# Performance work log

Measured on AMD Instinct MI355X. Metric: run time of the kernel, lower is better.

Reference implementation:

```python
import jax, jax.numpy as jnp
import numpy as np

NW = 30000   # window nodes
NE = 30000   # example nodes
E  = 480000  # edges per relation (avg degree 16)
H  = 512     # hidden_channels
L  = 4       # num_layers
SLOPE = 0.2
LAM = 0.5    # CSRA residual attention weight


def _segment_mean(x, idx, n):
    s = jax.ops.segment_sum(x, idx, num_segments=n)
    c = jax.ops.segment_sum(jnp.ones((idx.shape[0], 1), x.dtype), idx, num_segments=n)
    return s / jnp.maximum(c, 1.0)


def _sage(x_src, x_dst, edge, Wl, Wr, b, n_dst):
    # PyG SAGEConv: lin_l(mean_agg(x_j)) + lin_r(x_i)
    agg = _segment_mean(x_src[edge[0]], edge[1], n_dst)  # [n_dst, H]
    return agg @ Wl + b + x_dst @ Wr


def setup_inputs() -> dict:
    key = jax.random.key(0)
    ks = jax.random.split(key, 24)
    s = 0.02
    nrm = lambda k, shape: (jax.random.normal(k, shape, jnp.float32) * s)
    return {
        "x_window": jax.random.normal(ks[0], (NW, 1949), jnp.float32),
        "x_example": jax.random.normal(ks[1], (NE, 100), jnp.float32),
        "edge_near": jax.random.randint(ks[2], (2, E), 0, NW, jnp.int32),
        "edge_close": jax.random.randint(ks[3], (2, E), 0, NE, jnp.int32),
        "edge_refer": jax.random.randint(ks[4], (2, E), 0, NW, jnp.int32),  # src=example, dst=window
        "W_win": nrm(ks[5], (1949, H)),
        "W_exp": nrm(ks[6], (100, H)),
        "W_post": nrm(ks[7], (H, H)),
        "W_ey": nrm(ks[8], (250, H)),
        "Wl_near": nrm(ks[9], (L, H, H)),
        "Wr_near": nrm(ks[10], (L, H, H)),
        "b_near": jnp.zeros((L, H), jnp.float32),
        "Wl_close": nrm(ks[11], (L, H, H)),
        "Wr_close": nrm(ks[12], (L, H, H)),
        "b_close": jnp.zeros((L, H), jnp.float32),
        "Wl_refer": nrm(ks[13], (L, H, H)),
        "Wr_refer": nrm(ks[14], (L, H, H)),
        "b_refer": jnp.zeros((L, H), jnp.float32),
        "w_pool": nrm(ks[15], (H,)),
        "W_lin": nrm(ks[16], (H, 100)),
        "b_lin": jnp.zeros((100,), jnp.float32),
    }


def reference(x_window, x_example, edge_near, edge_close, edge_refer,
              W_win, W_exp, W_post, W_ey,
              Wl_near, Wr_near, b_near,
              Wl_close, Wr_close, b_close,
              Wl_refer, Wr_refer, b_refer,
              w_pool, W_lin, b_lin):
    lrelu = lambda x: jax.nn.leaky_relu(x, SLOPE)
    post = lambda h: lrelu(lrelu(h) @ W_post)  # LeakyReLU -> Linear -> LeakyReLU

    h_exp = post(x_example @ W_exp)            # [NE, H]
    h_win = post(x_window @ W_win)             # [NW, H]
    # example_y is computed in the original but dropped by HeteroConv (no conv
    # targets it); compute for faithfulness, unused.
    _example_y = h_exp[:, -250:] @ W_ey

    for l in range(L):
        o_near = _sage(h_win, h_win, edge_near, Wl_near[l], Wr_near[l], b_near[l], NW)
        o_refer = _sage(h_exp, h_win, edge_refer, Wl_refer[l], Wr_refer[l], b_refer[l], NW)
        o_close = _sage(h_exp, h_exp, edge_close, Wl_close[l], Wr_close[l], b_close[l], NE)
        h_win = lrelu((o_near + o_refer) * 0.5)  # HeteroConv aggr='mean' over 2 relations
        h_exp = lrelu(o_close)

    # CSRA-style pooling: residual attention over 'refer' edges into window nodes
    src, dst = edge_refer[0], edge_refer[1]
    score = h_exp @ w_pool                      # [NE]
    s = score[src]                              # [E]
    m = jax.ops.segment_max(s, dst, num_segments=NW)
    ex = jnp.exp(s - m[dst])
    z = jax.ops.segment_sum(ex, dst, num_segments=NW)
    att = ex / jnp.maximum(z[dst], 1e-12)
    pooled = jax.ops.segment_sum(att[:, None] * h_exp[src], dst, num_segments=NW)
    out = h_win + LAM * pooled                  # [NW, H]
    return out @ W_lin + b_lin                  # [NW, 100]
```

## Files before the change

### kernel.cpp

```cpp
#include <hip/hip_runtime.h>
#include <hip/hip_bf16.h>
#include <cstdint>
#include <cstddef>

#define NW 30000
#define NE 30000
#define EE 480000
#define HD 512
#define NL 4
#define SLOPE 0.2f
#define LAM 0.5f
#define ROWP 30080
#define MT 235
#define WHH ((size_t)HD * HD)

typedef short short8 __attribute__((ext_vector_type(8)));
typedef float f32x4 __attribute__((ext_vector_type(4)));

static __device__ __forceinline__ float lrelu_f(float x){
    return fmaxf(x, 0.f) + SLOPE * fminf(x, 0.f);
}
static __device__ __forceinline__ short f2bf(float f){
    uint32_t u = __builtin_bit_cast(uint32_t, f);
    u += 0x7FFFu + ((u >> 16) & 1u);
    return (short)(u >> 16);
}
static __device__ __forceinline__ float bf2f(short s){
    uint32_t u = ((uint32_t)(uint16_t)s) << 16;
    return __builtin_bit_cast(float, u);
}

typedef const __attribute__((address_space(1))) void* gas_t;
typedef __attribute__((address_space(3))) void* las_t;
static __device__ __forceinline__ void gload16(const void* g, void* l){
    __builtin_amdgcn_global_load_lds((gas_t)g, (las_t)l, 16, 0, 0);
}


__global__ void count3_kernel(const int* __restrict__ dn, const int* __restrict__ dr,
                              const int* __restrict__ dc, int* __restrict__ deg){
    int z = blockIdx.y;
    const int* dst = (z == 0) ? dn : ((z == 1) ? dr : dc);
    int e = blockIdx.x * 256 + threadIdx.x;
    if (e < EE) atomicAdd(&deg[z * 30000 + dst[e]], 1);
}

__global__ void scan3_kernel(const int* __restrict__ deg, int* __restrict__ off3){
    const int* dg = deg + blockIdx.x * 30000;
    int* off = off3 + blockIdx.x * (NW + 1);
    int n = 30000;
    __shared__ int tmp[1024];
    int t = threadIdx.x;
    int carry = 0;
    if (t == 0) off[0] = 0;
    for (int base = 0; base < n; base += 1024){
        int v = (base + t < n) ? dg[base + t] : 0;
        tmp[t] = v; __syncthreads();
        for (int d = 1; d < 1024; d <<= 1){
            int add = (t >= d) ? tmp[t - d] : 0;
            __syncthreads();
            tmp[t] += add;
            __syncthreads();
        }
        if (base + t < n) off[base + t + 1] = tmp[t] + carry;
        carry += tmp[1023];
        __syncthreads();
    }
}

__global__ void fill3_kernel(const int* __restrict__ sn, const int* __restrict__ dn,
                             const int* __restrict__ sr, const int* __restrict__ dr,
                             const int* __restrict__ sc, const int* __restrict__ dc,
                             int* __restrict__ cur, const int* __restrict__ off3,
                             int* __restrict__ el3){
    int z = blockIdx.y;
    const int* src = (z == 0) ? sn : ((z == 1) ? sr : sc);
    const int* dst = (z == 0) ? dn : ((z == 1) ? dr : dc);
    const int* off = off3 + z * (NW + 1);
    int* el = el3 + (size_t)z * EE;
    int e = blockIdx.x * 256 + threadIdx.x;
    if (e < EE){
        int d = dst[e];
        int p = atomicAdd(&cur[z * 30000 + d], 1);
        el[off[d] + p] = src[e];
    }
}


__global__ __launch_bounds__(256)
void transpose_bf_kernel(const float* __restrict__ in, short* __restrict__ out,
                         int K, int N, int Kpad){
    __shared__ float tile[32][33];
    int kbase = blockIdx.y * 32, nbase = blockIdx.x * 32;
    int tx = threadIdx.x & 31, ty = threadIdx.x >> 5;
    #pragma unroll
    for (int r = 0; r < 4; ++r){
        int k = kbase + ty + r * 8;
        float v = 0.f;
        if (k < K) v = in[(size_t)k * N + nbase + tx];
        tile[ty + r * 8][tx] = v;
    }
    __syncthreads();
    #pragma unroll
    for (int r = 0; r < 4; ++r){
        int n = nbase + ty + r * 8;
        int k = kbase + tx;
        if (k < Kpad) out[(size_t)n * Kpad + k] = f2bf(tile[tx][ty + r * 8]);
    }
}


__global__ __launch_bounds__(256)
void transpose_all_kernel(const float* __restrict__ Wln, const float* __restrict__ Wlr,
                          const float* __restrict__ Wlc, const float* __restrict__ Wrc,
                          const float* __restrict__ Wrn, const float* __restrict__ Wrr,
                          const float* __restrict__ Wpost, short* __restrict__ outT){
    __shared__ float tile[32][33];
    int z = blockIdx.z;
    const float* a; const float* b = nullptr;
    if (z < 4) a = Wln + (size_t)z * WHH;
    else if (z < 8) a = Wlr + (size_t)(z - 4) * WHH;
    else if (z < 12) a = Wlc + (size_t)(z - 8) * WHH;
    else if (z < 16) a = Wrc + (size_t)(z - 12) * WHH;
    else if (z < 20){ a = Wrn + (size_t)(z - 16) * WHH; b = Wrr + (size_t)(z - 16) * WHH; }
    else a = Wpost;
    short* outp = outT + (size_t)z * WHH;
    int kbase = blockIdx.y * 32, nbase = blockIdx.x * 32;
    int tx = threadIdx.x & 31, ty = threadIdx.x >> 5;
    #pragma unroll
    for (int r = 0; r < 4; ++r){
        int k = kbase + ty + r * 8;
        float v = a[(size_t)k * HD + nbase + tx];
        if (b) v += b[(size_t)k * HD + nbase + tx];
        tile[ty + r * 8][tx] = v;
    }
    __syncthreads();
    #pragma unroll
    for (int r = 0; r < 4; ++r){
        int n = nbase + ty + r * 8;
        outp[(size_t)n * HD + kbase + tx] = f2bf(tile[tx][ty + r * 8]);
    }
}

__global__ void addf_kernel(const float* __restrict__ a, const float* __restrict__ b,
                            float* __restrict__ o, int n){
    int i = blockIdx.x * 256 + threadIdx.x;
    if (i < n) o[i] = a[i] + b[i];
}


__global__ __launch_bounds__(256)
void conv_xw_kernel(const float* __restrict__ x, short* __restrict__ o){
    int idx = blockIdx.x * 256 + threadIdx.x;
    if (idx >= 30000 * 244) return;
    int row = idx / 244, c8 = idx - row * 244;
    int base = c8 * 8;
    short8 v = {};
    const float* xp = x + (size_t)row * 1949 + base;
    if (base + 8 <= 1949){
        f32x4 a = *(const f32x4*)xp;
        f32x4 bq = *(const f32x4*)(xp + 4);
        #pragma unroll
        for (int j = 0; j < 4; ++j){ v[j] = f2bf(a[j]); v[j + 4] = f2bf(bq[j]); }
    } else {
        #pragma unroll
        for (int j = 0; j < 8; ++j) if (base + j < 1949) v[j] = f2bf(xp[j]);
    }
    *(short8*)(o + (size_t)row * 1952 + base) = v;
}


__global__ __launch_bounds__(256)
void conv_xe_kernel(const float* __restrict__ x, short* __restrict__ o){
    int idx = blockIdx.x * 256 + threadIdx.x;
    if (idx >= ROWP * 16) return;
    int row = idx >> 4, c8 = idx & 15;
    int base = c8 * 8;
    short8 v = {};
    if (row < 30000){
        const float* xp = x + (size_t)row * 100 + base;
        #pragma unroll
        for (int j = 0; j < 8; ++j) if (base + j < 100) v[j] = f2bf(xp[j]);
    }
    *(short8*)(o + (size_t)row * 128 + base) = v;
}


__global__ __launch_bounds__(256)
void seg_mean3_kernel(const short* __restrict__ hw, const short* __restrict__ he,
                      const int* __restrict__ off3, const int* __restrict__ el3,
                      short* __restrict__ aggA, short* __restrict__ aggB, short* __restrict__ aggC){
    int slot = blockIdx.x * 4 + (threadIdx.x >> 6);
    int lane = threadIdx.x & 63;
    if (slot >= 3 * NW) return;
    int seg = slot / NW;
    int dst = slot - seg * NW;
    const short* h = (seg == 0) ? hw : he;
    const int* off = off3 + seg * (NW + 1);
    const int* el = el3 + (size_t)seg * EE;
    short* out = (seg == 0) ? aggA : ((seg == 1) ? aggB : aggC);
    int s0 = off[dst], s1 = off[dst + 1];
    float acc[8] = {};
    int e = s0;
    for (; e + 8 <= s1; e += 8){
        int idx[8];
        #pragma unroll
        for (int u = 0; u < 8; ++u) idx[u] = el[e + u];
        short8 v[8];
        #pragma unroll
        for (int u = 0; u < 8; ++u) v[u] = *(const short8*)(h + (size_t)idx[u] * HD + lane * 8);
        #pragma unroll
        for (int u = 0; u < 8; ++u)
            #pragma unroll
            for (int j = 0; j < 8; ++j) acc[j] += bf2f(v[u][j]);
    }
    for (; e < s1; ++e){
        short8 v = *(const short8*)(h + (size_t)el[e] * HD + lane * 8);
        #pragma unroll
        for (int j = 0; j < 8; ++j) acc[j] += bf2f(v[j]);
    }
    float inv = (s1 > s0) ? 1.0f / (float)(s1 - s0) : 0.0f;
    short8 o8;
    #pragma unroll
    for (int j = 0; j < 8; ++j) o8[j] = f2bf(acc[j] * inv);
    *(short8*)(out + (size_t)dst * HD + lane * 8) = o8;
}


template<int DUAL>
__global__ __launch_bounds__(256)
void mgemm2_kernel(
    const short* __restrict__ a00, const short* __restrict__ a01, const short* __restrict__ a02,
    const short* __restrict__ b00, const short* __restrict__ b01, const short* __restrict__ b02,
    const float* __restrict__ bias0, short* __restrict__ c160, float* __restrict__ c320,
    int np0, int kt0, int act0,
    const short* __restrict__ a10, const short* __restrict__ a11, const short* __restrict__ a12,
    const short* __restrict__ b10, const short* __restrict__ b11, const short* __restrict__ b12,
    const float* __restrict__ bias1, short* __restrict__ c161, float* __restrict__ c321,
    int np1, int kt1, int act1,
    int mreal){
    __shared__ short lds[24576];

    int nwg = gridDim.x, orig = blockIdx.x;
    int q = nwg >> 3, r = nwg & 7;
    int xcd = orig & 7, lid = orig >> 3;
    int logical = (xcd < r ? xcd * (q + 1) : r * (q + 1) + (xcd - r) * q) + lid;
    int mtile = logical >> 2, nc = logical & 3;
    int dsel, ml;
    if (DUAL){ dsel = mtile & 1; ml = mtile >> 1; } else { dsel = 0; ml = mtile; }

    const short* A0 = dsel ? a10 : a00;
    const short* A1 = dsel ? a11 : a01;
    const short* A2 = dsel ? a12 : a02;
    const short* B0 = dsel ? b10 : b00;
    const short* B1 = dsel ? b11 : b01;
    const short* B2 = dsel ? b12 : b02;
    const float* bias = dsel ? bias1 : bias0;
    short* C16 = dsel ? c161 : c160;
    float* C32 = dsel ? c321 : c320;
    const int np = dsel ? np1 : np0;
    const int kt = dsel ? kt1 : kt0;
    const int act = dsel ? act1 : act0;

    const int row0 = ml * 128, n0 = nc * 128;
    const int t = threadIdx.x, wid = t >> 6, lane = t & 63;
    const int wm = (wid >> 1) * 64, wn = (wid & 1) * 64;
    const int lg = lane >> 4, lr = lane & 15;
    f32x4 acc[4][4] = {};

    int rowi[2], ci[2];
    #pragma unroll
    for (int i = 0; i < 2; ++i){
        int sl = i * 256 + t;
        rowi[i] = sl >> 2;
        ci[i] = (sl & 3) ^ ((rowi[i] >> 1) & 3);
    }
    const int kpt = kt >> 5;
    const int nsteps = np * kpt;

    const short* Acur = A0;
    const short* Bcur = B0;
    int sk = 0, sp = 0, sbuf = 0;

    auto stage = [&](){
        int k0 = sk * 32;
        #pragma unroll
        for (int i = 0; i < 2; ++i){
            int ao = (row0 + rowi[i]) * kt + k0 + ci[i] * 8;
            gload16(Acur + ao, &lds[sbuf * 4096 + (i * 256 + wid * 64) * 8]);
        }
        #pragma unroll
        for (int i = 0; i < 2; ++i){
            int bo = (n0 + rowi[i]) * kt + k0 + ci[i] * 8;
            gload16(Bcur + bo, &lds[12288 + sbuf * 4096 + (i * 256 + wid * 64) * 8]);
        }
        sbuf = (sbuf == 2) ? 0 : sbuf + 1;
        if (++sk == kpt){
            sk = 0; ++sp;
            Acur = (sp == 1) ? A1 : A2;
            Bcur = (sp == 1) ? B1 : B2;
        }
    };
    auto compute = [&](int cb){
        const char* baseA = (const char*)(lds + cb * 4096);
        const char* baseB = (const char*)(lds + 12288 + cb * 4096);
        short8 af[4], bfr[4];
        #pragma unroll
        for (int f = 0; f < 4; ++f){
            int rowA = wm + f * 16 + lr;
            af[f] = *(const short8*)(baseA + rowA * 64 + ((lg ^ ((rowA >> 1) & 3)) << 4));
            int rowB = wn + f * 16 + lr;
            bfr[f] = *(const short8*)(baseB + rowB * 64 + ((lg ^ ((rowB >> 1) & 3)) << 4));
        }
        #pragma unroll
        for (int i = 0; i < 4; ++i)
            #pragma unroll
            for (int j = 0; j < 4; ++j)
                acc[i][j] = __builtin_amdgcn_mfma_f32_16x16x32_bf16(af[i], bfr[j], acc[i][j], 0, 0, 0);
    };

    stage();
    int cbuf = 0;
    for (int s = 0; s < nsteps; ++s){
        if (s + 1 < nsteps){
            stage();
            asm volatile("s_waitcnt vmcnt(4)" ::: "memory");
        } else {
            asm volatile("s_waitcnt vmcnt(0)" ::: "memory");
        }
        __builtin_amdgcn_s_barrier();
        __builtin_amdgcn_sched_barrier(0);
        compute(cbuf);
        cbuf = (cbuf == 2) ? 0 : cbuf + 1;
    }

    float bv[4];
    #pragma unroll
    for (int f = 0; f < 4; ++f) bv[f] = bias ? bias[n0 + wn + f * 16 + lr] : 0.f;
    #pragma unroll
    for (int i = 0; i < 4; ++i){
        #pragma unroll
        for (int r2 = 0; r2 < 4; ++r2){
            int gr = row0 + wm + i * 16 + lg * 4 + r2;
            #pragma unroll
            for (int j = 0; j < 4; ++j){
                int gc = n0 + wn + j * 16 + lr;
                float v = acc[i][j][r2] + bv[j];
                if (act == 2) v *= 0.5f;
                if (act) v = lrelu_f(v);
                C16[(size_t)gr * HD + gc] = f2bf(v);
                if (C32 && gr < mreal) C32[(size_t)gr * HD + gc] = v;
            }
        }
    }
}


__global__ __launch_bounds__(128)
void mgemm_af32_kernel(const float* __restrict__ A0, const short* __restrict__ B0,
                       short* __restrict__ C16, int M){
    constexpr int KT = 1952, KACT = 1949, KPT = KT / 32, NSTEPS = KPT, N = 512;
    __shared__ short ldsA[2][2048];
    __shared__ short ldsB[2][4096];
    int nwg = gridDim.x;
    int orig = blockIdx.x;
    int q = nwg >> 3, r = nwg & 7;
    int xcd = orig & 7, lid = orig >> 3;
    int logical = (xcd < r ? xcd * (q + 1) : r * (q + 1) + (xcd - r) * q) + lid;
    const int m0 = (logical >> 2) * 64, n0 = (logical & 3) * 128;
    const int t = threadIdx.x, wid = t >> 6, lane = t & 63;
    const int wn = wid * 64;
    const int lg = lane >> 4, lr = lane & 15;
    f32x4 acc[4][4] = {};
    int rowiA[2], ciA[2];
    #pragma unroll
    for (int i = 0; i < 2; ++i){
        int sl = i * 128 + t;
        rowiA[i] = sl >> 2;
        ciA[i] = (sl & 3) ^ ((rowiA[i] >> 1) & 3);
    }
    int rowiB[4], ciB[4];
    #pragma unroll
    for (int i = 0; i < 4; ++i){
        int sl = i * 128 + t;
        rowiB[i] = sl >> 2;
        ciB[i] = (sl & 3) ^ ((rowiB[i] >> 1) & 3);
    }
    f32x4 ra[2][2];
    auto stage_load = [&](int s){
        int k0 = s * 32;
        int bb = s & 1;
        #pragma unroll
        for (int i = 0; i < 2; ++i){
            int gr = m0 + rowiA[i];
            int gk = k0 + ciA[i] * 8;
            ra[i][0] = (f32x4){0,0,0,0};
            ra[i][1] = (f32x4){0,0,0,0};
            if (gr < M){
                const float* ap = A0 + (size_t)gr * KACT + gk;
                if (gk + 8 <= KACT){
                    ra[i][0] = *(const f32x4*)ap;
                    ra[i][1] = *(const f32x4*)(ap + 4);
                } else {
                    #pragma unroll
                    for (int j = 0; j < 8; ++j)
                        if (gk + j < KACT) ra[i][j >> 2][j & 3] = ap[j];
                }
            }
        }
        #pragma unroll
        for (int i = 0; i < 4; ++i)
            gload16(B0 + (size_t)(n0 + rowiB[i]) * KT + k0 + ciB[i] * 8,
                    &ldsB[bb][(i * 128 + wid * 64) * 8]);
    };
    auto stage_writeA = [&](int s){
        int bb = s & 1;
        #pragma unroll
        for (int i = 0; i < 2; ++i){
            short8 v;
            #pragma unroll
            for (int j = 0; j < 8; ++j) v[j] = f2bf(ra[i][j >> 2][j & 3]);
            *(short8*)&ldsA[bb][(i * 128 + t) * 8] = v;
        }
    };
    auto compute = [&](int s){
        int bb = s & 1;
        short8 af[4], bfr[4];
        #pragma unroll
        for (int f = 0; f < 4; ++f){
            int rowA = f * 16 + lr;
            af[f] = *(const short8*)((const char*)&ldsA[bb][0] + rowA * 64 + ((lg ^ ((rowA >> 1) & 3)) << 4));
            int rowB = wn + f * 16 + lr;
            bfr[f] = *(const short8*)((const char*)&ldsB[bb][0] + rowB * 64 + ((lg ^ ((rowB >> 1) & 3)) << 4));
        }
        #pragma unroll
        for (int i = 0; i < 4; ++i)
            #pragma unroll
            for (int j = 0; j < 4; ++j)
                acc[i][j] = __builtin_amdgcn_mfma_f32_16x16x32_bf16(af[i], bfr[j], acc[i][j], 0, 0, 0);
    };
    stage_load(0);
    stage_writeA(0);
    __syncthreads();
    for (int s = 0; s < NSTEPS; ++s){
        if (s + 1 < NSTEPS) stage_load(s + 1);
        compute(s);
        if (s + 1 < NSTEPS) stage_writeA(s + 1);
        __syncthreads();
    }
    #pragma unroll
    for (int i = 0; i < 4; ++i){
        #pragma unroll
        for (int r2 = 0; r2 < 4; ++r2){
            int gr = m0 + i * 16 + lg * 4 + r2;
            if (gr >= M) continue;
            #pragma unroll
            for (int j = 0; j < 4; ++j){
                int gc = n0 + wn + j * 16 + lr;
                C16[(size_t)gr * N + gc] = f2bf(lrelu_f(acc[i][j][r2]));
            }
        }
    }
}


__global__ __launch_bounds__(256)
void gemm_kernel(const float* __restrict__ A, const float* __restrict__ B,
                 const float* __restrict__ bias, float* __restrict__ C,
                 int M, int N, int K){
    const int BM = 128, BN = 64, BK = 16;
    __shared__ float As[BK][BM];
    __shared__ float Bs[BK][BN];
    int m0 = blockIdx.y * BM, n0 = blockIdx.x * BN;
    int t = threadIdx.x;
    int tx = t & 15, ty = t >> 4;
    float acc[8][4] = {};
    for (int k0 = 0; k0 < K; k0 += BK){
        #pragma unroll
        for (int i = 0; i < 2; ++i){
            int idx = i * 256 + t;
            int row = idx >> 2, kg = idx & 3;
            float4 v = make_float4(0,0,0,0);
            int gr = m0 + row, gk = k0 + kg * 4;
            if (gr < M && gk + 4 <= K)
                v = *reinterpret_cast<const float4*>(A + (size_t)gr * K + gk);
            As[kg*4+0][row] = v.x; As[kg*4+1][row] = v.y;
            As[kg*4+2][row] = v.z; As[kg*4+3][row] = v.w;
        }
        {
            int row = t >> 4, cg = t & 15;
            int gk = k0 + row, col = n0 + cg * 4;
            float4 v = make_float4(0,0,0,0);
            if (gk < K){
                if (col + 4 <= N){
                    v = *reinterpret_cast<const float4*>(B + (size_t)gk * N + col);
                } else {
                    float tp[4] = {0,0,0,0};
                    #pragma unroll
                    for (int j = 0; j < 4; ++j) if (col + j < N) tp[j] = B[(size_t)gk * N + col + j];
                    v = make_float4(tp[0], tp[1], tp[2], tp[3]);
                }
            }
            *reinterpret_cast<float4*>(&Bs[row][cg*4]) = v;
        }
        __syncthreads();
        #pragma unroll
        for (int k = 0; k < BK; ++k){
            float a[8], b[4];
            #pragma unroll
            for (int r = 0; r < 8; ++r) a[r] = As[k][ty*8 + r];
            #pragma unroll
            for (int c = 0; c < 4; ++c) b[c] = Bs[k][tx*4 + c];
            #pragma unroll
            for (int r = 0; r < 8; ++r)
                #pragma unroll
                for (int c = 0; c < 4; ++c)
                    acc[r][c] = fmaf(a[r], b[c], acc[r][c]);
        }
        __syncthreads();
    }
    #pragma unroll
    for (int r = 0; r < 8; ++r){
        int gr = m0 + ty*8 + r;
        if (gr >= M) continue;
        #pragma unroll
        for (int c = 0; c < 4; ++c){
            int gc = n0 + tx*4 + c;
            if (gc >= N) continue;
            C[(size_t)gr * N + gc] = acc[r][c] + bias[gc];
        }
    }
}


__global__ void score_kernel(const short* __restrict__ he, const float* __restrict__ w,
                             float* __restrict__ score){
    int row = blockIdx.x * 4 + (threadIdx.x >> 6);
    int lane = threadIdx.x & 63;
    if (row >= NE) return;
    float s = 0.f;
    #pragma unroll
    for (int j = 0; j < 8; ++j){
        int idx = lane + j * 64;
        s += bf2f(he[(size_t)row * HD + idx]) * w[idx];
    }
    #pragma unroll
    for (int off = 32; off > 0; off >>= 1) s += __shfl_down(s, off);
    if (lane == 0) score[row] = s;
}

__global__ __launch_bounds__(256)
void pool_kernel(const short* __restrict__ he, const float* __restrict__ hwf,
                 const float* __restrict__ score, const int* __restrict__ off,
                 const int* __restrict__ elist, float* __restrict__ outp){
    int dst = blockIdx.x * 4 + (threadIdx.x >> 6);
    int lane = threadIdx.x & 63;
    if (dst >= NW) return;
    int s0 = off[dst], s1 = off[dst + 1];
    float m = -INFINITY;
    for (int e = s0 + lane; e < s1; e += 64) m = fmaxf(m, score[elist[e]]);
    #pragma unroll
    for (int o = 1; o < 64; o <<= 1) m = fmaxf(m, __shfl_xor(m, o));
    float z = 0.f;
    for (int e = s0 + lane; e < s1; e += 64) z += expf(score[elist[e]] - m);
    #pragma unroll
    for (int o = 1; o < 64; o <<= 1) z += __shfl_xor(z, o);
    float zinv = 1.0f / fmaxf(z, 1e-12f);

    float acc[8] = {};
    int e = s0;
    for (; e + 4 <= s1; e += 4){
        int idx[4]; float at[4];
        #pragma unroll
        for (int u = 0; u < 4; ++u) idx[u] = elist[e + u];
        #pragma unroll
        for (int u = 0; u < 4; ++u) at[u] = expf(score[idx[u]] - m) * zinv;
        #pragma unroll
        for (int u = 0; u < 4; ++u){
            short8 v = *(const short8*)(he + (size_t)idx[u] * HD + lane * 8);
            #pragma unroll
            for (int k = 0; k < 8; ++k) acc[k] += at[u] * bf2f(v[k]);
        }
    }
    for (; e < s1; ++e){
        int src = elist[e];
        float at = expf(score[src] - m) * zinv;
        short8 v = *(const short8*)(he + (size_t)src * HD + lane * 8);
        #pragma unroll
        for (int k = 0; k < 8; ++k) acc[k] += at * bf2f(v[k]);
    }
    f32x4 h0 = *(const f32x4*)(hwf + (size_t)dst * HD + lane * 8);
    f32x4 h1 = *(const f32x4*)(hwf + (size_t)dst * HD + lane * 8 + 4);
    f32x4 o0, o1;
    #pragma unroll
    for (int k = 0; k < 4; ++k){ o0[k] = h0[k] + LAM * acc[k]; o1[k] = h1[k] + LAM * acc[k+4]; }
    *(f32x4*)(outp + (size_t)dst * HD + lane * 8) = o0;
    *(f32x4*)(outp + (size_t)dst * HD + lane * 8 + 4) = o1;
}


extern "C" void kernel_launch(void* const* d_in, const int* in_sizes, int n_in,
                              void* d_out, int out_size, void* d_ws, size_t ws_size,
                              hipStream_t stream){
    const float* x_window = (const float*)d_in[0];
    const float* x_example= (const float*)d_in[1];
    const int*   e_near   = (const int*)d_in[2];
    const int*   e_close  = (const int*)d_in[3];
    const int*   e_refer  = (const int*)d_in[4];
    const float* W_win    = (const float*)d_in[5];
    const float* W_exp    = (const float*)d_in[6];
    const float* W_post   = (const float*)d_in[7];
    const float* Wl_near  = (const float*)d_in[9];
    const float* Wr_near  = (const float*)d_in[10];
    const float* b_near   = (const float*)d_in[11];
    const float* Wl_close = (const float*)d_in[12];
    const float* Wr_close = (const float*)d_in[13];
    const float* b_close  = (const float*)d_in[14];
    const float* Wl_refer = (const float*)d_in[15];
    const float* Wr_refer = (const float*)d_in[16];
    const float* b_refer  = (const float*)d_in[17];
    const float* w_pool   = (const float*)d_in[18];
    const float* W_lin    = (const float*)d_in[19];
    const float* b_lin    = (const float*)d_in[20];
    float* out = (float*)d_out;
    (void)in_sizes; (void)n_in; (void)out_size;

    char* w = (char*)d_ws;
    size_t o = 0;
    auto alloc = [&](size_t bytes)->char*{
        char* p = w + o;
        o += (bytes + 255) & ~(size_t)255;
        return p;
    };
    const size_t HBH = (size_t)ROWP * HD * 2;

    short* h16[2][2];
    h16[0][0] = (short*)alloc(HBH); h16[0][1] = (short*)alloc(HBH);
    h16[1][0] = (short*)alloc(HBH); h16[1][1] = (short*)alloc(HBH);
    short* aggA = (short*)alloc(HBH);
    short* aggB = (short*)alloc(HBH);
    short* aggC = (short*)alloc(HBH);
    float* hwf  = (float*)alloc((size_t)NW * HD * 4);
    float* pooled = (float*)alloc((size_t)NW * HD * 4);
    short* xe16   = (short*)alloc((size_t)ROWP * 128 * 2);
    short* WwinT  = (short*)alloc((size_t)HD * 1952 * 2);
    short* WexpT  = (short*)alloc((size_t)HD * 128 * 2);
    short* WT     = (short*)alloc((size_t)21 * WHH * 2);
    short* WlnT = WT;
    short* WlrT = WT + 4 * WHH;
    short* WlcT = WT + 8 * WHH;
    short* WrcT = WT + 12 * WHH;
    short* WcbT = WT + 16 * WHH;
    short* WpostT = WT + 20 * WHH;
    float* bsum   = (float*)alloc((size_t)NL * HD * 4);
    float* score  = (float*)alloc((size_t)NE * 4);
    int* degcur = (int*)alloc((size_t)6 * 30000 * 4);
    int* deg3 = degcur;
    int* cur3 = degcur + 90000;
    int* off3 = (int*)alloc((size_t)3 * (NW + 1) * 4);
    int* el3  = (int*)alloc((size_t)3 * EE * 4);
    int* off_r = off3 + (NW + 1);

    const size_t XWB = (size_t)ROWP * 1952 * 2;
    bool haveXW16 = false;
    short* xw16 = nullptr;
    size_t rem = (ws_size > o) ? ws_size - o : 0;
    if (rem >= XWB + 256){
        xw16 = (short*)alloc(XWB);
        haveXW16 = true;
    }

    const int* src_n = e_near;  const int* dst_n = e_near + EE;
    const int* src_c = e_close; const int* dst_c = e_close + EE;
    const int* src_r = e_refer; const int* dst_r = e_refer + EE;

    hipMemsetAsync(degcur, 0, (size_t)6 * 30000 * 4, stream);
    int eg = (EE + 255) / 256;
    hipLaunchKernelGGL(count3_kernel, dim3(eg, 3), dim3(256), 0, stream, dst_n, dst_r, dst_c, deg3);
    hipLaunchKernelGGL(scan3_kernel, dim3(3), dim3(1024), 0, stream, deg3, off3);
    hipLaunchKernelGGL(fill3_kernel, dim3(eg, 3), dim3(256), 0, stream,
                       src_n, dst_n, src_r, dst_r, src_c, dst_c, cur3, off3, el3);

    hipLaunchKernelGGL(transpose_bf_kernel, dim3(16, 61, 1), dim3(256), 0, stream,
                       W_win, WwinT, 1949, HD, 1952);
    hipLaunchKernelGGL(transpose_bf_kernel, dim3(16, 4, 1), dim3(256), 0, stream,
                       W_exp, WexpT, 100, HD, 128);
    hipLaunchKernelGGL(transpose_all_kernel, dim3(16, 16, 21), dim3(256), 0, stream,
                       Wl_near, Wl_refer, Wl_close, Wr_close, Wr_near, Wr_refer, W_post, WT);
    hipLaunchKernelGGL(addf_kernel, dim3((NL * HD + 255) / 256), dim3(256), 0, stream,
                       b_near, b_refer, bsum, NL * HD);
    hipLaunchKernelGGL(conv_xe_kernel, dim3((ROWP * 16 + 255) / 256), dim3(256), 0, stream,
                       x_example, xe16);
    if (haveXW16)
        hipLaunchKernelGGL(conv_xw_kernel, dim3((30000 * 244 + 255) / 256), dim3(256), 0, stream,
                           x_window, xw16);

    const short* z16 = xe16;
    const float* zf = nullptr;

    hipLaunchKernelGGL((mgemm2_kernel<0>), dim3(MT * 4), dim3(256), 0, stream,
        xe16, z16, z16, WexpT, z16, z16, zf, aggA, (float*)nullptr, 1, 128, 1,
        z16, z16, z16, z16, z16, z16, zf, (short*)nullptr, (float*)nullptr, 0, 32, 0, 30000);
    if (haveXW16){
        hipLaunchKernelGGL((mgemm2_kernel<0>), dim3(MT * 4), dim3(256), 0, stream,
            xw16, z16, z16, WwinT, z16, z16, zf, aggB, (float*)nullptr, 1, 1952, 1,
            z16, z16, z16, z16, z16, z16, zf, (short*)nullptr, (float*)nullptr, 0, 32, 0, 30000);
    } else {
        hipLaunchKernelGGL(mgemm_af32_kernel, dim3(4 * ((NW + 63) / 64)), dim3(128), 0, stream,
                           x_window, WwinT, aggB, NW);
    }
    hipLaunchKernelGGL((mgemm2_kernel<1>), dim3(2 * MT * 4), dim3(256), 0, stream,
        aggA, z16, z16, WpostT, z16, z16, zf, h16[1][0], (float*)nullptr, 1, 512, 1,
        aggB, z16, z16, WpostT, z16, z16, zf, h16[0][0], (float*)nullptr, 1, 512, 1, 30000);

    for (int l = 0; l < NL; ++l){
        int cur = l & 1, nxt = cur ^ 1;
        const short* wl_n = WlnT + (size_t)l * WHH;
        const short* wl_r = WlrT + (size_t)l * WHH;
        const short* wl_c = WlcT + (size_t)l * WHH;
        const short* wr_c = WrcT + (size_t)l * WHH;
        const short* wcb  = WcbT + (size_t)l * WHH;
        const float* bs   = bsum + (size_t)l * HD;
        const float* bc   = b_close + (size_t)l * HD;
        bool last = (l == NL - 1);

        hipLaunchKernelGGL(seg_mean3_kernel, dim3((3 * NW + 3) / 4), dim3(256), 0, stream,
                           h16[0][cur], h16[1][cur], off3, el3, aggA, aggB, aggC);
        hipLaunchKernelGGL((mgemm2_kernel<1>), dim3(2 * MT * 4), dim3(256), 0, stream,
            aggA, aggB, h16[0][cur], wl_n, wl_r, wcb, bs, h16[0][nxt],
            last ? hwf : (float*)nullptr, 3, 512, 2,
            aggC, h16[1][cur], z16, wl_c, wr_c, z16, bc, h16[1][nxt],
            (float*)nullptr, 2, 512, 1, 30000);
    }
    int fin = NL & 1;

    hipLaunchKernelGGL(score_kernel, dim3((NE + 3) / 4), dim3(256), 0, stream,
                       h16[1][fin], w_pool, score);
    hipLaunchKernelGGL(pool_kernel, dim3((NW + 3) / 4), dim3(256), 0, stream,
                       h16[1][fin], hwf, score, off_r, el3 + (size_t)EE, pooled);

    hipLaunchKernelGGL(gemm_kernel, dim3(2, (NW + 127) / 128), dim3(256), 0, stream,
                       pooled, W_lin, b_lin, out, NW, 100, HD);
}
```

Before: 1.763 ms.

## Overlap self-weight GEMMs with segment-mean gather in one fused launch

The self-term products (h_win·Wcb and h_exp·Wr_close) move into a new kernel that runs GEMM blocks and segment-mean gather blocks side by side in the same grid. This lets the compute-bound and memory-bound work share the GPU at once. The main layer GEMM then uses fewer K panels and adds the precomputed bf16 self-term in its epilogue. The mgemm2 pipeline is also changed to prefetch two stages ahead, and s_setprio is raised around the MFMA work. The cost is extra bf16 intermediate buffers, an added rounding step on the self-term, and a possible race risk in the 3-buffer prefetch now that the trailing barrier is gone.

```diff
diff --git a/kernel.cpp b/kernel.cpp
--- a/kernel.cpp
+++ b/kernel.cpp
@@ -187,43 +187,121 @@
 
 
 __global__ __launch_bounds__(256)
-void seg_mean3_kernel(const short* __restrict__ hw, const short* __restrict__ he,
-                      const int* __restrict__ off3, const int* __restrict__ el3,
-                      short* __restrict__ aggA, short* __restrict__ aggB, short* __restrict__ aggC){
-    int slot = blockIdx.x * 4 + (threadIdx.x >> 6);
-    int lane = threadIdx.x & 63;
-    if (slot >= 3 * NW) return;
-    int seg = slot / NW;
-    int dst = slot - seg * NW;
-    const short* h = (seg == 0) ? hw : he;
-    const int* off = off3 + seg * (NW + 1);
-    const int* el = el3 + (size_t)seg * EE;
-    short* out = (seg == 0) ? aggA : ((seg == 1) ? aggB : aggC);
-    int s0 = off[dst], s1 = off[dst + 1];
-    float acc[8] = {};
-    int e = s0;
-    for (; e + 8 <= s1; e += 8){
-        int idx[8];
-        #pragma unroll
-        for (int u = 0; u < 8; ++u) idx[u] = el[e + u];
-        short8 v[8];
-        #pragma unroll
-        for (int u = 0; u < 8; ++u) v[u] = *(const short8*)(h + (size_t)idx[u] * HD + lane * 8);
-        #pragma unroll
-        for (int u = 0; u < 8; ++u)
-            #pragma unroll
-            for (int j = 0; j < 8; ++j) acc[j] += bf2f(v[u][j]);
-    }
-    for (; e < s1; ++e){
-        short8 v = *(const short8*)(h + (size_t)el[e] * HD + lane * 8);
-        #pragma unroll
-        for (int j = 0; j < 8; ++j) acc[j] += bf2f(v[j]);
-    }
-    float inv = (s1 > s0) ? 1.0f / (float)(s1 - s0) : 0.0f;
-    short8 o8;
-    #pragma unroll
-    for (int j = 0; j < 8; ++j) o8[j] = f2bf(acc[j] * inv);
-    *(short8*)(out + (size_t)dst * HD + lane * 8) = o8;
+void fused_self_seg_kernel(const short* __restrict__ hw, const short* __restrict__ he,
+                           const short* __restrict__ Wcb, const short* __restrict__ Wrc,
+                           short* __restrict__ Zw16, short* __restrict__ Ze16,
+                           const int* __restrict__ off3, const int* __restrict__ el3,
+                           short* __restrict__ aggA, short* __restrict__ aggB,
+                           short* __restrict__ aggC, int ngemm){
+    __shared__ short lds[16384];
+    int t = threadIdx.x;
+    if ((int)blockIdx.x < ngemm){
+        int logical = blockIdx.x;
+        int mtile = logical >> 2, nc = logical & 3;
+        int dsel = mtile & 1, ml = mtile >> 1;
+        const short* A = dsel ? he : hw;
+        const short* B = dsel ? Wrc : Wcb;
+        short* C16 = dsel ? Ze16 : Zw16;
+        const int row0 = ml * 128, n0 = nc * 128;
+        const int wid = t >> 6, lane = t & 63;
+        const int wm = (wid >> 1) * 64, wn = (wid & 1) * 64;
+        const int lg = lane >> 4, lr = lane & 15;
+        f32x4 acc[4][4] = {};
+        int rowi[2], ci[2];
+        #pragma unroll
+        for (int i = 0; i < 2; ++i){
+            int sl = i * 256 + t;
+            rowi[i] = sl >> 2;
+            ci[i] = (sl & 3) ^ ((rowi[i] >> 1) & 3);
+        }
+        auto stage = [&](int s){
+            int k0 = s * 32, bb = s & 1;
+            #pragma unroll
+            for (int i = 0; i < 2; ++i)
+                gload16(A + (size_t)(row0 + rowi[i]) * HD + k0 + ci[i] * 8,
+                        &lds[bb * 4096 + (i * 256 + wid * 64) * 8]);
+            #pragma unroll
+            for (int i = 0; i < 2; ++i)
+                gload16(B + (size_t)(n0 + rowi[i]) * HD + k0 + ci[i] * 8,
+                        &lds[8192 + bb * 4096 + (i * 256 + wid * 64) * 8]);
+        };
+        auto compute = [&](int bb){
+            const char* baseA = (const char*)(lds + bb * 4096);
+            const char* baseB = (const char*)(lds + 8192 + bb * 4096);
+            short8 af[4], bfr[4];
+            #pragma unroll
+            for (int f = 0; f < 4; ++f){
+                int rowA = wm + f * 16 + lr;
+                af[f] = *(const short8*)(baseA + rowA * 64 + ((lg ^ ((rowA >> 1) & 3)) << 4));
+                int rowB = wn + f * 16 + lr;
+                bfr[f] = *(const short8*)(baseB + rowB * 64 + ((lg ^ ((rowB >> 1) & 3)) << 4));
+            }
+            #pragma unroll
+            for (int i = 0; i < 4; ++i)
+                #pragma unroll
+                for (int j = 0; j < 4; ++j)
+                    acc[i][j] = __builtin_amdgcn_mfma_f32_16x16x32_bf16(af[i], bfr[j], acc[i][j], 0, 0, 0);
+        };
+        stage(0);
+        for (int s = 0; s < 16; ++s){
+            if (s + 1 < 16){
+                stage(s + 1);
+                asm volatile("s_waitcnt vmcnt(4)" ::: "memory");
+            } else {
+                asm volatile("s_waitcnt vmcnt(0)" ::: "memory");
+            }
+            __builtin_amdgcn_s_barrier();
+            __builtin_amdgcn_sched_barrier(0);
+            compute(s & 1);
+            asm volatile("s_waitcnt lgkmcnt(0)" ::: "memory");
+            __builtin_amdgcn_sched_barrier(0);
+            __builtin_amdgcn_s_barrier();
+        }
+        #pragma unroll
+        for (int i = 0; i < 4; ++i)
+            #pragma unroll
+            for (int r2 = 0; r2 < 4; ++r2){
+                int gr = row0 + wm + i * 16 + lg * 4 + r2;
+                #pragma unroll
+                for (int j = 0; j < 4; ++j)
+                    C16[(size_t)gr * HD + n0 + wn + j * 16 + lr] = f2bf(acc[i][j][r2]);
+            }
+    } else {
+        int slot = (blockIdx.x - ngemm) * 4 + (t >> 6);
+        int lane = t & 63;
+        if (slot >= 3 * NW) return;
+        int seg = slot / NW;
+        int dst = slot - seg * NW;
+        const short* h = (seg == 0) ? hw : he;
+        const int* off = off3 + seg * (NW + 1);
+        const int* el = el3 + (size_t)seg * EE;
+        short* outp = (seg == 0) ? aggA : ((seg == 1) ? aggB : aggC);
+        int s0 = off[dst], s1 = off[dst + 1];
+        float acc[8] = {};
+        int e = s0;
+        for (; e + 8 <= s1; e += 8){
+            int idx[8];
+            #pragma unroll
+            for (int u = 0; u < 8; ++u) idx[u] = el[e + u];
+            short8 v[8];
+            #pragma unroll
+            for (int u = 0; u < 8; ++u) v[u] = *(const short8*)(h + (size_t)idx[u] * HD + lane * 8);
+            #pragma unroll
+            for (int u = 0; u < 8; ++u)
+                #pragma unroll
+                for (int j = 0; j < 8; ++j) acc[j] += bf2f(v[u][j]);
+        }
+        for (; e < s1; ++e){
+            short8 v = *(const short8*)(h + (size_t)el[e] * HD + lane * 8);
+            #pragma unroll
+            for (int j = 0; j < 8; ++j) acc[j] += bf2f(v[j]);
+        }
+        float inv = (s1 > s0) ? 1.0f / (float)(s1 - s0) : 0.0f;
+        short8 o8;
+        #pragma unroll
+        for (int j = 0; j < 8; ++j) o8[j] = f2bf(acc[j] * inv);
+        *(short8*)(outp + (size_t)dst * HD + lane * 8) = o8;
+    }
 }
 
 
@@ -233,11 +311,11 @@
     const short* __restrict__ a00, const short* __restrict__ a01, const short* __restrict__ a02,
     const short* __restrict__ b00, const short* __restrict__ b01, const short* __restrict__ b02,
     const float* __restrict__ bias0, short* __restrict__ c160, float* __restrict__ c320,
-    int np0, int kt0, int act0,
+    const short* __restrict__ cin0, int np0, int kt0, int act0,
     const short* __restrict__ a10, const short* __restrict__ a11, const short* __restrict__ a12,
     const short* __restrict__ b10, const short* __restrict__ b11, const short* __restrict__ b12,
     const float* __restrict__ bias1, short* __restrict__ c161, float* __restrict__ c321,
-    int np1, int kt1, int act1,
+    const short* __restrict__ cin1, int np1, int kt1, int act1,
     int mreal){
     __shared__ short lds[24576];
 
@@ -258,6 +336,7 @@
     const float* bias = dsel ? bias1 : bias0;
     short* C16 = dsel ? c161 : c160;
     float* C32 = dsel ? c321 : c320;
+    const short* cin = dsel ? cin1 : cin0;
     const int np = dsel ? np1 : np0;
     const int kt = dsel ? kt1 : kt0;
     const int act = dsel ? act1 : act0;
@@ -320,17 +399,19 @@
     };
 
     stage();
+    stage();
     int cbuf = 0;
     for (int s = 0; s < nsteps; ++s){
         if (s + 1 < nsteps){
-            stage();
             asm volatile("s_waitcnt vmcnt(4)" ::: "memory");
         } else {
             asm volatile("s_waitcnt vmcnt(0)" ::: "memory");
         }
         __builtin_amdgcn_s_barrier();
-        __builtin_amdgcn_sched_barrier(0);
+        if (s + 2 < nsteps) stage();
+        __builtin_amdgcn_s_setprio(1);
         compute(cbuf);
+        __builtin_amdgcn_s_setprio(0);
         cbuf = (cbuf == 2) ? 0 : cbuf + 1;
     }
 
@@ -346,6 +427,7 @@
             for (int j = 0; j < 4; ++j){
                 int gc = n0 + wn + j * 16 + lr;
                 float v = acc[i][j][r2] + bv[j];
+                if (cin) v += bf2f(cin[(size_t)gr * HD + gc]);
                 if (act == 2) v *= 0.5f;
                 if (act) v = lrelu_f(v);
                 C16[(size_t)gr * HD + gc] = f2bf(v);
@@ -640,6 +722,8 @@
     short* aggA = (short*)alloc(HBH);
     short* aggB = (short*)alloc(HBH);
     short* aggC = (short*)alloc(HBH);
+    short* Zw16 = (short*)alloc(HBH);
+    short* Ze16 = (short*)alloc(HBH);
     float* hwf  = (float*)alloc((size_t)NW * HD * 4);
     float* pooled = (float*)alloc((size_t)NW * HD * 4);
     short* xe16   = (short*)alloc((size_t)ROWP * 128 * 2);
@@ -696,23 +780,26 @@
                            x_window, xw16);
 
     const short* z16 = xe16;
+    const short* zc = nullptr;
     const float* zf = nullptr;
 
     hipLaunchKernelGGL((mgemm2_kernel<0>), dim3(MT * 4), dim3(256), 0, stream,
-        xe16, z16, z16, WexpT, z16, z16, zf, aggA, (float*)nullptr, 1, 128, 1,
-        z16, z16, z16, z16, z16, z16, zf, (short*)nullptr, (float*)nullptr, 0, 32, 0, 30000);
+        xe16, z16, z16, WexpT, z16, z16, zf, aggA, (float*)nullptr, zc, 1, 128, 1,
+        z16, z16, z16, z16, z16, z16, zf, (short*)nullptr, (float*)nullptr, zc, 0, 32, 0, 30000);
     if (haveXW16){
         hipLaunchKernelGGL((mgemm2_kernel<0>), dim3(MT * 4), dim3(256), 0, stream,
-            xw16, z16, z16, WwinT, z16, z16, zf, aggB, (float*)nullptr, 1, 1952, 1,
-            z16, z16, z16, z16, z16, z16, zf, (short*)nullptr, (float*)nullptr, 0, 32, 0, 30000);
+            xw16, z16, z16, WwinT, z16, z16, zf, aggB, (float*)nullptr, zc, 1, 1952, 1,
+            z16, z16, z16, z16, z16, z16, zf, (short*)nullptr, (float*)nullptr, zc, 0, 32, 0, 30000);
     } else {
         hipLaunchKernelGGL(mgemm_af32_kernel, dim3(4 * ((NW + 63) / 64)), dim3(128), 0, stream,
                            x_window, WwinT, aggB, NW);
     }
     hipLaunchKernelGGL((mgemm2_kernel<1>), dim3(2 * MT * 4), dim3(256), 0, stream,
-        aggA, z16, z16, WpostT, z16, z16, zf, h16[1][0], (float*)nullptr, 1, 512, 1,
-        aggB, z16, z16, WpostT, z16, z16, zf, h16[0][0], (float*)nullptr, 1, 512, 1, 30000);
-
+        aggA, z16, z16, WpostT, z16, z16, zf, h16[1][0], (float*)nullptr, zc, 1, 512, 1,
+        aggB, z16, z16, WpostT, z16, z16, zf, h16[0][0], (float*)nullptr, zc, 1, 512, 1, 30000);
+
+    const int NGEMM = 2 * MT * 4;
+    const int NSEG  = (3 * NW + 3) / 4;
     for (int l = 0; l < NL; ++l){
         int cur = l & 1, nxt = cur ^ 1;
         const short* wl_n = WlnT + (size_t)l * WHH;
@@ -724,13 +811,14 @@
         const float* bc   = b_close + (size_t)l * HD;
         bool last = (l == NL - 1);
 
-        hipLaunchKernelGGL(seg_mean3_kernel, dim3((3 * NW + 3) / 4), dim3(256), 0, stream,
-                           h16[0][cur], h16[1][cur], off3, el3, aggA, aggB, aggC);
+        hipLaunchKernelGGL(fused_self_seg_kernel, dim3(NGEMM + NSEG), dim3(256), 0, stream,
+                           h16[0][cur], h16[1][cur], wcb, wr_c, Zw16, Ze16,
+                           off3, el3, aggA, aggB, aggC, NGEMM);
         hipLaunchKernelGGL((mgemm2_kernel<1>), dim3(2 * MT * 4), dim3(256), 0, stream,
-            aggA, aggB, h16[0][cur], wl_n, wl_r, wcb, bs, h16[0][nxt],
-            last ? hwf : (float*)nullptr, 3, 512, 2,
-            aggC, h16[1][cur], z16, wl_c, wr_c, z16, bc, h16[1][nxt],
-            (float*)nullptr, 2, 512, 1, 30000);
+            aggA, aggB, z16, wl_n, wl_r, z16, bs, h16[0][nxt],
+            last ? hwf : (float*)nullptr, Zw16, 2, 512, 2,
+            aggC, z16, z16, wl_c, z16, z16, bc, h16[1][nxt],
+            (float*)nullptr, Ze16, 1, 512, 1, 30000);
     }
     int fin = NL & 1;
 
```

Result: slower. 2.279 ms (+29.3%).
